# Kernel optimization log

Hardware: AMD Instinct MI355X
Metric: run time of the kernel (lower is better)

Reference implementation:

```python
import jax, jax.numpy as jnp
import numpy as np

B, C, H, W, K = 4, 32, 192, 192, 3
BETA = 15.0   # soft-max temperature used by the repo's Morphology module
EPS = 1e-5    # BatchNorm eps
KK = K * K


def _window_taps(x, dil):
    """Zero-padded dilated KxK window taps, stacked on axis 0 -> (KK, B, C, H, W).
    Matches nn.Unfold(kernel_size=K, dilation=dil, padding=dil*(K//2))."""
    p = dil * (K // 2)
    xp = jnp.pad(x, ((0, 0), (0, 0), (p, p), (p, p)))
    return jnp.stack(
        [xp[:, :, i * dil:i * dil + H, j * dil:j * dil + W]
         for i in range(K) for j in range(K)], axis=0)


def _w_taps(w):
    # (C, K, K) -> (KK, 1, C, 1, 1) aligned with tap order i*K+j
    return w.reshape(C, KK).T[:, None, :, None, None]


def soft_dilate(x, w, dil):
    v = _window_taps(x, dil) + _w_taps(w)          # (KK,B,C,H,W)
    return jax.nn.logsumexp(BETA * v, axis=0) / BETA


def soft_erode(x, w, dil):
    v = _w_taps(w) - _window_taps(x, dil)
    return -(jax.nn.logsumexp(BETA * v, axis=0) / BETA)


def batchnorm(x, gamma, beta):
    mu = jnp.mean(x, axis=(0, 2, 3), keepdims=True)
    var = jnp.var(x, axis=(0, 2, 3), keepdims=True)
    xn = (x - mu) * jax.lax.rsqrt(var + EPS)
    return xn * gamma[None, :, None, None] + beta[None, :, None, None]


def setup_inputs() -> dict:
    key = jax.random.key(0)
    k1, k2, k3, k4 = jax.random.split(key, 4)
    return {
        "x": jax.random.normal(k1, (B, C, H, W), jnp.float32),
        "wd": jax.random.normal(k2, (4, C, K, K), jnp.float32) * 0.1,
        "we": jax.random.normal(k3, (4, C, K, K), jnp.float32) * 0.1,
        "gs": jnp.ones((4, C), jnp.float32),
        "bs": jnp.zeros((4, C), jnp.float32),
        "Wc": jax.random.normal(k4, (C, 4 * C), jnp.float32) * (1.0 / np.sqrt(4 * C)),
        "g": jnp.ones((C,), jnp.float32),
        "b": jnp.zeros((C,), jnp.float32),
    }


def reference(x, wd, we, gs, bs, Wc, g, b):
    branches = []
    for i in range(4):                      # fixed set of dilation factors 1..4
        d = i + 1
        y = soft_dilate(x, wd[i], d)        # soft morphological dilation
        y = soft_erode(y, we[i], d)         # then erosion => closing
        y = jax.nn.relu(batchnorm(y, gs[i], bs[i]))
        branches.append(y)
    xc = jnp.concatenate(branches, axis=1)  # (B, 4C, H, W)
    y = jnp.einsum('bihw,oi->bohw', xc, Wc) # 1x1 conv, no bias
    y = jax.nn.relu(batchnorm(y, g, b))
    return y                                 # Dropout2d is identity in eval
```

## Files before the change

### kernel.cpp

```cpp
#include <hip/hip_runtime.h>
#include <hip/hip_bf16.h>

#define B_   4
#define C_   32
#define H_   192
#define W_   192
#define HW_  (H_ * W_)
#define EPS_ 1e-5f

#define SCALE_IN  21.640425613334453f
#define SCALE_OUT 0.046209812037329687f

#define SPW 52
#define SQW 44

#define NP1 (128 * 576)
#define NP2 (32 * 4 * 144)

__device__ __forceinline__ float bf2f(unsigned short u) {
    return __uint_as_float((unsigned int)u << 16);
}
__device__ __forceinline__ unsigned short f2bf(float f) {
    const unsigned int u = __float_as_uint(f);
    return (unsigned short)((u + 0x7fffu + ((u >> 16) & 1u)) >> 16);
}

__device__ float          g_cw[2304];
__device__ float          g_Wt[4096];
__device__ float          g_stats[320];
__device__ float          g_p1[2 * NP1];
__device__ float          g_p2[2 * NP2];
__device__ __attribute__((aligned(16))) unsigned short g_E[(size_t)4 * B_ * C_ * HW_];
__device__ __attribute__((aligned(16))) float          g_Y[(size_t)B_ * C_ * HW_];

__global__ void prep_k(const float* __restrict__ wd, const float* __restrict__ we,
                       const float* __restrict__ Wc) {
    for (int i = threadIdx.x; i < 2304; i += 256) {
        const float v = (i < 1152) ? wd[i] : we[i - 1152];
        g_cw[i] = exp2f(SCALE_IN * v);
    }
    for (int i = threadIdx.x; i < 4096; i += 256) {
        const int ci = i >> 5;
        const int k  = i & 31;
        g_Wt[i] = Wc[(size_t)k * 128 + ci];
    }
}

template<int D>
__device__ __forceinline__ void morph_branch(int b, int c, int h0, int w0,
                                             int slotbase,
                                             const float* __restrict__ sP,
                                             float* __restrict__ sQ) {
    constexpr int QE   = 32 + 2 * D;
    constexpr int QEG  = (QE + 3) / 4;
    constexpr int UNITS = QE * QEG;
    constexpr int POFF = 8 - 2 * D;
    constexpr int AB   = POFF & ~3;
    constexpr int OFF  = POFF & 3;
    constexpr int NR   = (OFF + 2 * D + 4 + 3) / 4;
    constexpr int NR3  = (2 * D + 4 + 3) / 4;
    constexpr int br   = D - 1;

    const int tid = threadIdx.x;
    const int cb  = (br * C_ + c) * 9;

    {
        float cd[9];
#pragma unroll
        for (int k = 0; k < 9; k++) cd[k] = g_cw[cb + k];

#pragma unroll
        for (int it = 0; it < 2; ++it) {
            const int unit = tid + it * 256;
            if (unit < UNITS) {
                const int qi = unit / QEG;
                const int qj = (unit - qi * QEG) * 4;
                float a0 = 0.f, a1 = 0.f, a2 = 0.f, a3 = 0.f;
#pragma unroll
                for (int i = 0; i < 3; i++) {
                    const float* rp = &sP[(qi + 8 + (i - 2) * D) * SPW + qj + AB];
                    float buf[NR * 4];
#pragma unroll
                    for (int r = 0; r < NR; r++)
                        *(float4*)&buf[r * 4] = *(const float4*)&rp[r * 4];
#pragma unroll
                    for (int j = 0; j < 3; j++) {
                        const float wgt = cd[i * 3 + j];
                        a0 = fmaf(wgt, buf[OFF + j * D + 0], a0);
                        a1 = fmaf(wgt, buf[OFF + j * D + 1], a1);
                        a2 = fmaf(wgt, buf[OFF + j * D + 2], a2);
                        a3 = fmaf(wgt, buf[OFF + j * D + 3], a3);
                    }
                }
                float q0 = __builtin_amdgcn_rcpf(a0);
                float q1 = __builtin_amdgcn_rcpf(a1);
                float q2 = __builtin_amdgcn_rcpf(a2);
                float q3 = __builtin_amdgcn_rcpf(a3);
                const int hq = h0 - D + qi;
                const int wq = w0 - D + qj;
                const bool rowo = (hq < 0) || (hq >= H_);
                q0 = (rowo || (wq + 0 < 0) || (wq + 0 >= W_)) ? 1.0f : q0;
                q1 = (rowo || (wq + 1 < 0) || (wq + 1 >= W_)) ? 1.0f : q1;
                q2 = (rowo || (wq + 2 < 0) || (wq + 2 >= W_)) ? 1.0f : q2;
                q3 = (rowo || (wq + 3 < 0) || (wq + 3 >= W_)) ? 1.0f : q3;
                *(float4*)&sQ[qi * SQW + qj] = make_float4(q0, q1, q2, q3);
            }
        }
    }
    __syncthreads();

    {
        float ce[9];
#pragma unroll
        for (int k = 0; k < 9; k++) ce[k] = g_cw[1152 + cb + k];

        const int oi = tid >> 3;
        const int oj = (tid & 7) * 4;
        float t0 = 0.f, t1 = 0.f, t2 = 0.f, t3 = 0.f;
#pragma unroll
        for (int i = 0; i < 3; i++) {
            const float* rq = &sQ[(oi + i * D) * SQW + oj];
            float buf[NR3 * 4];
#pragma unroll
            for (int r = 0; r < NR3; r++)
                *(float4*)&buf[r * 4] = *(const float4*)&rq[r * 4];
#pragma unroll
            for (int j = 0; j < 3; j++) {
                const float wgt = ce[i * 3 + j];
                t0 = fmaf(wgt, buf[j * D + 0], t0);
                t1 = fmaf(wgt, buf[j * D + 1], t1);
                t2 = fmaf(wgt, buf[j * D + 2], t2);
                t3 = fmaf(wgt, buf[j * D + 3], t3);
            }
        }
        const float e0 = -SCALE_OUT * log2f(t0);
        const float e1 = -SCALE_OUT * log2f(t1);
        const float e2 = -SCALE_OUT * log2f(t2);
        const float e3 = -SCALE_OUT * log2f(t3);

        ushort4 r4;
        r4.x = f2bf(e0); r4.y = f2bf(e1); r4.z = f2bf(e2); r4.w = f2bf(e3);
        *(ushort4*)&g_E[(((size_t)br * B_ + b) * C_ + c) * HW_
                        + (size_t)(h0 + oi) * W_ + w0 + oj] = r4;

        float s1 = e0 + e1 + e2 + e3;
        float s2 = e0 * e0 + e1 * e1 + e2 * e2 + e3 * e3;
#pragma unroll
        for (int off = 32; off >= 1; off >>= 1) {
            s1 += __shfl_down(s1, off, 64);
            s2 += __shfl_down(s2, off, 64);
        }
        if ((tid & 63) == 0) {
            const int slot = (br * C_ + c) * 576 + slotbase + (tid >> 6);
            g_p1[slot]       = s1;
            g_p1[NP1 + slot] = s2;
        }
    }
    __syncthreads();
}

__global__ __launch_bounds__(256) void morph_k(const float* __restrict__ x) {
    __shared__ float sP[48 * SPW];
    __shared__ float sQ[40 * SQW];
    const int tile = blockIdx.x;
    const int c    = blockIdx.y;
    const int b    = blockIdx.z;
    const int th   = tile / 6;
    const int tw   = tile - th * 6;
    const int h0   = th * 32, w0 = tw * 32;

    const float* xm = x + (size_t)(b * C_ + c) * HW_;
    for (int idx = threadIdx.x; idx < 48 * SPW; idx += 256) {
        const int r  = idx / SPW, q = idx - r * SPW;
        const int ih = h0 - 8 + r, iw = w0 - 8 + q;
        const int ihc = min(max(ih, 0), H_ - 1);
        const int iwc = min(max(iw, 0), W_ - 1);
        const float xv = xm[ihc * W_ + iwc];
        const bool inb = (ih == ihc) && (iw == iwc);
        sP[idx] = inb ? exp2f(SCALE_IN * xv) : 1.0f;
    }
    __syncthreads();

    const int slotbase = (b * 36 + tile) * 4;
    morph_branch<1>(b, c, h0, w0, slotbase, sP, sQ);
    morph_branch<2>(b, c, h0, w0, slotbase, sP, sQ);
    morph_branch<3>(b, c, h0, w0, slotbase, sP, sQ);
    morph_branch<4>(b, c, h0, w0, slotbase, sP, sQ);
}

__global__ __launch_bounds__(256) void fin1_k(const float* __restrict__ gs,
                                              const float* __restrict__ bs) {
    const int chan = blockIdx.x;
    const int base = chan * 576;
    float s1 = 0.0f, s2 = 0.0f;
    for (int i = threadIdx.x; i < 576; i += 256) {
        s1 += g_p1[base + i];
        s2 += g_p1[NP1 + base + i];
    }
#pragma unroll
    for (int off = 32; off >= 1; off >>= 1) {
        s1 += __shfl_down(s1, off, 64);
        s2 += __shfl_down(s2, off, 64);
    }
    __shared__ float l1[4], l2[4];
    const int lane = threadIdx.x & 63;
    const int wv   = threadIdx.x >> 6;
    if (lane == 0) { l1[wv] = s1; l2[wv] = s2; }
    __syncthreads();
    if (threadIdx.x == 0) {
        const float S1 = l1[0] + l1[1] + l1[2] + l1[3];
        const float S2 = l2[0] + l2[1] + l2[2] + l2[3];
        const float N  = (float)(B_ * HW_);
        const float mu = S1 / N;
        const float va = fmaxf(S2 / N - mu * mu, 0.0f);
        const float sc = gs[chan] * rsqrtf(va + EPS_);
        g_stats[chan]       = sc;
        g_stats[128 + chan] = bs[chan] - mu * sc;
    }
}

__global__ __launch_bounds__(256) void conv_k(void) {
    const int og = blockIdx.y;
    const int b  = blockIdx.z;
    const int p  = blockIdx.x * 256 + threadIdx.x;

    float acc[8];
#pragma unroll
    for (int k = 0; k < 8; k++) acc[k] = 0.0f;

#pragma unroll 4
    for (int ci = 0; ci < 128; ci++) {
        const int br = ci >> 5;
        const int c  = ci & 31;
        const unsigned short eu = g_E[(((size_t)br * B_ + b) * C_ + c) * HW_ + p];
        float v = bf2f(eu);
        v = fmaxf(fmaf(v, g_stats[ci], g_stats[128 + ci]), 0.0f);
        const float* wr = &g_Wt[ci * 32 + og * 8];
#pragma unroll
        for (int k = 0; k < 8; k++) acc[k] = fmaf(v, wr[k], acc[k]);
    }

    float* Yp = g_Y + ((size_t)b * C_ + og * 8) * HW_ + p;
#pragma unroll
    for (int k = 0; k < 8; k++) Yp[(size_t)k * HW_] = acc[k];

    __shared__ float l1[8][4], l2[8][4];
    const int lane = threadIdx.x & 63;
    const int wv   = threadIdx.x >> 6;
#pragma unroll
    for (int k = 0; k < 8; k++) {
        float s1 = acc[k];
        float s2 = acc[k] * acc[k];
#pragma unroll
        for (int off = 32; off >= 1; off >>= 1) {
            s1 += __shfl_down(s1, off, 64);
            s2 += __shfl_down(s2, off, 64);
        }
        if (lane == 0) { l1[k][wv] = s1; l2[k][wv] = s2; }
    }
    __syncthreads();
    if (threadIdx.x < 8) {
        const int k = threadIdx.x;
        const int chan = og * 8 + k;
        const int slot = chan * (B_ * 144) + b * 144 + blockIdx.x;
        g_p2[slot]       = l1[k][0] + l1[k][1] + l1[k][2] + l1[k][3];
        g_p2[NP2 + slot] = l2[k][0] + l2[k][1] + l2[k][2] + l2[k][3];
    }
}

__global__ __launch_bounds__(256) void fin2_k(const float* __restrict__ g,
                                              const float* __restrict__ bb) {
    const int chan = blockIdx.x;
    const int base = chan * (B_ * 144);
    float s1 = 0.0f, s2 = 0.0f;
    for (int i = threadIdx.x; i < B_ * 144; i += 256) {
        s1 += g_p2[base + i];
        s2 += g_p2[NP2 + base + i];
    }
#pragma unroll
    for (int off = 32; off >= 1; off >>= 1) {
        s1 += __shfl_down(s1, off, 64);
        s2 += __shfl_down(s2, off, 64);
    }
    __shared__ float l1[4], l2[4];
    const int lane = threadIdx.x & 63;
    const int wv   = threadIdx.x >> 6;
    if (lane == 0) { l1[wv] = s1; l2[wv] = s2; }
    __syncthreads();
    if (threadIdx.x == 0) {
        const float S1 = l1[0] + l1[1] + l1[2] + l1[3];
        const float S2 = l2[0] + l2[1] + l2[2] + l2[3];
        const float N  = (float)(B_ * HW_);
        const float mu = S1 / N;
        const float va = fmaxf(S2 / N - mu * mu, 0.0f);
        const float sc = g[chan] * rsqrtf(va + EPS_);
        g_stats[256 + chan] = sc;
        g_stats[288 + chan] = bb[chan] - mu * sc;
    }
}

__global__ __launch_bounds__(256) void final_k(float* __restrict__ out) {
    const int c = blockIdx.y;
    const int b = blockIdx.z;
    const size_t base = (size_t)(b * C_ + c) * HW_ + (blockIdx.x * 256 + threadIdx.x) * 4;
    const float sc = g_stats[256 + c];
    const float sh = g_stats[288 + c];
    const float4 v = *(const float4*)&g_Y[base];
    float4 r;
    r.x = fmaxf(v.x * sc + sh, 0.0f);
    r.y = fmaxf(v.y * sc + sh, 0.0f);
    r.z = fmaxf(v.z * sc + sh, 0.0f);
    r.w = fmaxf(v.w * sc + sh, 0.0f);
    *(float4*)&out[base] = r;
}

extern "C" void kernel_launch(void* const* d_in, const int* in_sizes, int n_in,
                              void* d_out, int out_size, void* d_ws, size_t ws_size,
                              hipStream_t stream) {
    const float* x  = (const float*)d_in[0];
    const float* wd = (const float*)d_in[1];
    const float* we = (const float*)d_in[2];
    const float* gs = (const float*)d_in[3];
    const float* bs = (const float*)d_in[4];
    const float* Wc = (const float*)d_in[5];
    const float* g  = (const float*)d_in[6];
    const float* bb = (const float*)d_in[7];

    prep_k<<<1, 256, 0, stream>>>(wd, we, Wc);
    morph_k<<<dim3(36, C_, B_), 256, 0, stream>>>(x);
    fin1_k<<<128, 256, 0, stream>>>(gs, bs);
    conv_k<<<dim3(HW_ / 256, 4, B_), 256, 0, stream>>>();
    fin2_k<<<32, 256, 0, stream>>>(g, bb);
    final_k<<<dim3(HW_ / 1024, C_, B_), 256, 0, stream>>>((float*)d_out);
}
```

Before: 116.4 us.

## Store conv output as bf16, process two pixels per thread, shrink LDS pitch

The conv kernel now reads two packed bf16 inputs per load and keeps two pixel accumulators per thread, halving the grid. The intermediate conv output is written as bf16 instead of fp32, and the final BN/ReLU kernel reads it with 16-byte loads covering eight pixels per thread. This is meant to cut global memory traffic for the intermediate tensor and reduce per-pixel load overhead. The shared-memory row pitches in the morphology kernel also shrink from 52/44 to 48/40, which may change bank-conflict behaviour. The cost is bf16 rounding of the pre-BN conv output, which slightly reduces accuracy.

New measurement: 101.2 us. 1.15x faster.

```diff
diff --git a/kernel.cpp b/kernel.cpp
--- a/kernel.cpp
+++ b/kernel.cpp
@@ -11,11 +11,11 @@
 #define SCALE_IN  21.640425613334453f
 #define SCALE_OUT 0.046209812037329687f
 
-#define SPW 52
-#define SQW 44
+#define SPW 48
+#define SQW 40
 
 #define NP1 (128 * 576)
-#define NP2 (32 * 4 * 144)
+#define NP2 (32 * 288)
 
 __device__ __forceinline__ float bf2f(unsigned short u) {
     return __uint_as_float((unsigned int)u << 16);
@@ -31,7 +31,7 @@
 __device__ float          g_p1[2 * NP1];
 __device__ float          g_p2[2 * NP2];
 __device__ __attribute__((aligned(16))) unsigned short g_E[(size_t)4 * B_ * C_ * HW_];
-__device__ __attribute__((aligned(16))) float          g_Y[(size_t)B_ * C_ * HW_];
+__device__ __attribute__((aligned(16))) unsigned short g_Yb[(size_t)B_ * C_ * HW_];
 
 __global__ void prep_k(const float* __restrict__ wd, const float* __restrict__ we,
                        const float* __restrict__ Wc) {
@@ -170,14 +170,14 @@
     const int h0   = th * 32, w0 = tw * 32;
 
     const float* xm = x + (size_t)(b * C_ + c) * HW_;
-    for (int idx = threadIdx.x; idx < 48 * SPW; idx += 256) {
-        const int r  = idx / SPW, q = idx - r * SPW;
+    for (int idx = threadIdx.x; idx < 48 * 48; idx += 256) {
+        const int r  = idx / 48, q = idx - r * 48;
         const int ih = h0 - 8 + r, iw = w0 - 8 + q;
         const int ihc = min(max(ih, 0), H_ - 1);
         const int iwc = min(max(iw, 0), W_ - 1);
         const float xv = xm[ihc * W_ + iwc];
         const bool inb = (ih == ihc) && (iw == iwc);
-        sP[idx] = inb ? exp2f(SCALE_IN * xv) : 1.0f;
+        sP[r * SPW + q] = inb ? exp2f(SCALE_IN * xv) : 1.0f;
     }
     __syncthreads();
 
@@ -222,35 +222,46 @@
 __global__ __launch_bounds__(256) void conv_k(void) {
     const int og = blockIdx.y;
     const int b  = blockIdx.z;
-    const int p  = blockIdx.x * 256 + threadIdx.x;
-
-    float acc[8];
-#pragma unroll
-    for (int k = 0; k < 8; k++) acc[k] = 0.0f;
-
-#pragma unroll 4
+    const int p  = (blockIdx.x * 256 + threadIdx.x) * 2;
+
+    float acc0[8], acc1[8];
+#pragma unroll
+    for (int k = 0; k < 8; k++) { acc0[k] = 0.0f; acc1[k] = 0.0f; }
+
+#pragma unroll 8
     for (int ci = 0; ci < 128; ci++) {
         const int br = ci >> 5;
         const int c  = ci & 31;
-        const unsigned short eu = g_E[(((size_t)br * B_ + b) * C_ + c) * HW_ + p];
-        float v = bf2f(eu);
-        v = fmaxf(fmaf(v, g_stats[ci], g_stats[128 + ci]), 0.0f);
+        const unsigned int eu =
+            *(const unsigned int*)&g_E[(((size_t)br * B_ + b) * C_ + c) * HW_ + p];
+        float v0 = __uint_as_float(eu << 16);
+        float v1 = __uint_as_float(eu & 0xffff0000u);
+        const float sc = g_stats[ci], sh = g_stats[128 + ci];
+        v0 = fmaxf(fmaf(v0, sc, sh), 0.0f);
+        v1 = fmaxf(fmaf(v1, sc, sh), 0.0f);
         const float* wr = &g_Wt[ci * 32 + og * 8];
 #pragma unroll
-        for (int k = 0; k < 8; k++) acc[k] = fmaf(v, wr[k], acc[k]);
-    }
-
-    float* Yp = g_Y + ((size_t)b * C_ + og * 8) * HW_ + p;
-#pragma unroll
-    for (int k = 0; k < 8; k++) Yp[(size_t)k * HW_] = acc[k];
+        for (int k = 0; k < 8; k++) {
+            acc0[k] = fmaf(v0, wr[k], acc0[k]);
+            acc1[k] = fmaf(v1, wr[k], acc1[k]);
+        }
+    }
+
+    unsigned short* Yp = g_Yb + ((size_t)b * C_ + og * 8) * HW_ + p;
+#pragma unroll
+    for (int k = 0; k < 8; k++) {
+        const unsigned int pack =
+            (unsigned int)f2bf(acc0[k]) | ((unsigned int)f2bf(acc1[k]) << 16);
+        *(unsigned int*)&Yp[(size_t)k * HW_] = pack;
+    }
 
     __shared__ float l1[8][4], l2[8][4];
     const int lane = threadIdx.x & 63;
     const int wv   = threadIdx.x >> 6;
 #pragma unroll
     for (int k = 0; k < 8; k++) {
-        float s1 = acc[k];
-        float s2 = acc[k] * acc[k];
+        float s1 = acc0[k] + acc1[k];
+        float s2 = acc0[k] * acc0[k] + acc1[k] * acc1[k];
 #pragma unroll
         for (int off = 32; off >= 1; off >>= 1) {
             s1 += __shfl_down(s1, off, 64);
@@ -262,7 +273,7 @@
     if (threadIdx.x < 8) {
         const int k = threadIdx.x;
         const int chan = og * 8 + k;
-        const int slot = chan * (B_ * 144) + b * 144 + blockIdx.x;
+        const int slot = chan * 288 + b * 72 + blockIdx.x;
         g_p2[slot]       = l1[k][0] + l1[k][1] + l1[k][2] + l1[k][3];
         g_p2[NP2 + slot] = l2[k][0] + l2[k][1] + l2[k][2] + l2[k][3];
     }
@@ -271,9 +282,9 @@
 __global__ __launch_bounds__(256) void fin2_k(const float* __restrict__ g,
                                               const float* __restrict__ bb) {
     const int chan = blockIdx.x;
-    const int base = chan * (B_ * 144);
+    const int base = chan * 288;
     float s1 = 0.0f, s2 = 0.0f;
-    for (int i = threadIdx.x; i < B_ * 144; i += 256) {
+    for (int i = threadIdx.x; i < 288; i += 256) {
         s1 += g_p2[base + i];
         s2 += g_p2[NP2 + base + i];
     }
@@ -302,16 +313,23 @@
 __global__ __launch_bounds__(256) void final_k(float* __restrict__ out) {
     const int c = blockIdx.y;
     const int b = blockIdx.z;
-    const size_t base = (size_t)(b * C_ + c) * HW_ + (blockIdx.x * 256 + threadIdx.x) * 4;
+    const size_t base = (size_t)(b * C_ + c) * HW_ + (blockIdx.x * 256 + threadIdx.x) * 8;
     const float sc = g_stats[256 + c];
     const float sh = g_stats[288 + c];
-    const float4 v = *(const float4*)&g_Y[base];
-    float4 r;
-    r.x = fmaxf(v.x * sc + sh, 0.0f);
-    r.y = fmaxf(v.y * sc + sh, 0.0f);
-    r.z = fmaxf(v.z * sc + sh, 0.0f);
-    r.w = fmaxf(v.w * sc + sh, 0.0f);
-    *(float4*)&out[base] = r;
+    const uint4 u = *(const uint4*)&g_Yb[base];
+
+    float4 r0, r1;
+    r0.x = fmaxf(fmaf(__uint_as_float(u.x << 16),        sc, sh), 0.0f);
+    r0.y = fmaxf(fmaf(__uint_as_float(u.x & 0xffff0000u), sc, sh), 0.0f);
+    r0.z = fmaxf(fmaf(__uint_as_float(u.y << 16),        sc, sh), 0.0f);
+    r0.w = fmaxf(fmaf(__uint_as_float(u.y & 0xffff0000u), sc, sh), 0.0f);
+    r1.x = fmaxf(fmaf(__uint_as_float(u.z << 16),        sc, sh), 0.0f);
+    r1.y = fmaxf(fmaf(__uint_as_float(u.z & 0xffff0000u), sc, sh), 0.0f);
+    r1.z = fmaxf(fmaf(__uint_as_float(u.w << 16),        sc, sh), 0.0f);
+    r1.w = fmaxf(fmaf(__uint_as_float(u.w & 0xffff0000u), sc, sh), 0.0f);
+
+    *(float4*)&out[base]     = r0;
+    *(float4*)&out[base + 4] = r1;
 }
 
 extern "C" void kernel_launch(void* const* d_in, const int* in_sizes, int n_in,
@@ -329,7 +347,7 @@
     prep_k<<<1, 256, 0, stream>>>(wd, we, Wc);
     morph_k<<<dim3(36, C_, B_), 256, 0, stream>>>(x);
     fin1_k<<<128, 256, 0, stream>>>(gs, bs);
-    conv_k<<<dim3(HW_ / 256, 4, B_), 256, 0, stream>>>();
+    conv_k<<<dim3(HW_ / 512, 4, B_), 256, 0, stream>>>();
     fin2_k<<<32, 256, 0, stream>>>(g, bb);
-    final_k<<<dim3(HW_ / 1024, C_, B_), 256, 0, stream>>>((float*)d_out);
-}
+    final_k<<<dim3(HW_ / 2048, C_, B_), 256, 0, stream>>>((float*)d_out);
+}
```
